# Optimization experiments

Hardware: AMD Instinct MI355X
Metric: run time of the kernel (lower is better)

Reference implementation:

```python
import jax, jax.numpy as jnp
import numpy as np
import math

B, Hs, Ws, C, NH, PP = 4, 32, 32, 1024, 16, 128
N = Hs * Ws
HD = C // NH
MAX_REL = 32
ROPE_THETA = 10000.0


def _gelu(t):
    return jax.nn.gelu(t, approximate=False)  # torch nn.GELU default (erf)


def _rope(x):
    # x: [B, nh, N, hd]; interleaved even/odd rotation as in _apply_rope
    hd = x.shape[-1]
    inv_freq = 1.0 / (ROPE_THETA ** (jnp.arange(0, hd, 2, dtype=jnp.float32) / hd))
    pos = jnp.arange(x.shape[-2], dtype=jnp.float32)
    ang = pos[:, None] * inv_freq[None, :]  # [N, hd/2]
    sin, cos = jnp.sin(ang), jnp.cos(ang)
    x1, x2 = x[..., 0::2], x[..., 1::2]
    return jnp.stack([x1 * cos - x2 * sin, x2 * cos + x1 * sin], axis=-1).reshape(x.shape)


def _rel_bias(table):
    # static index computation (numpy), gather from learned table -> [1, NH, N, N]
    coords = np.arange(Hs)
    cy, cx = np.meshgrid(coords, coords, indexing='ij')
    cf = np.stack([cy.reshape(-1), cx.reshape(-1)])  # [2, N]
    rel = cf[:, :, None] - cf[:, None, :]            # [2, N, N]
    idx = (rel[0] + MAX_REL - 1) * (2 * MAX_REL - 1) + (rel[1] + MAX_REL - 1)
    return table[jnp.asarray(idx.reshape(-1))].reshape(N, N, NH).transpose(2, 0, 1)[None]


def setup_inputs() -> dict:
    key = jax.random.key(0)
    ks = iter(jax.random.split(key, 40))
    def w(shape, s=0.02):
        return jax.random.normal(next(ks), shape, jnp.float32) * s
    return dict(
        x=jax.random.normal(next(ks), (B, N, C), jnp.float32),
        plucker=jax.random.normal(next(ks), (B, Hs, Ws, 6), jnp.float32),
        w_qkv=w((C, 3 * C)), w_self_proj=w((C, C)), b_self_proj=jnp.zeros((C,), jnp.float32),
        pl_w1=w((6, 2 * PP)), pl_b1=jnp.zeros((2 * PP,), jnp.float32),
        pl_w2=w((2 * PP, PP)), pl_b2=jnp.zeros((PP,), jnp.float32),
        pl_w3=w((PP, PP)), pl_b3=jnp.zeros((PP,), jnp.float32),
        w_cq=w((C, C)), w_pk=w((PP, C)), w_pv=w((PP, C)),
        w_cross_proj=w((C, C)), b_cross_proj=jnp.zeros((C,), jnp.float32),
        ray_dir_bias=w((NH,)),
        ds_w1=w((6, 4 * NH)), ds_b1=jnp.zeros((4 * NH,), jnp.float32),
        ds_w2=w((4 * NH, NH)), ds_b2=jnp.zeros((NH,), jnp.float32),
        gb_w1=w((2 * PP, C // 2)), gb_b1=jnp.zeros((C // 2,), jnp.float32),
        gb_w2=w((C // 2, NH)), gb_b2=jnp.zeros((NH,), jnp.float32),
        rel_table=w(((2 * MAX_REL - 1) ** 2, NH)),
        gfe_w1=w((C + PP, C)), gfe_b1=jnp.zeros((C,), jnp.float32),
        gfe_w2=w((C, C)), gfe_b2=jnp.zeros((C,), jnp.float32),
    )


def reference(x, plucker, w_qkv, w_self_proj, b_self_proj,
              pl_w1, pl_b1, pl_w2, pl_b2, pl_w3, pl_b3,
              w_cq, w_pk, w_pv, w_cross_proj, b_cross_proj,
              ray_dir_bias, ds_w1, ds_b1, ds_w2, ds_b2,
              gb_w1, gb_b1, gb_w2, gb_b2, rel_table,
              gfe_w1, gfe_b1, gfe_w2, gfe_b2):
    scale = HD ** (-0.5)
    pl_flat = plucker.reshape(B, N, 6)

    # ---- self attention with RoPE + relative position bias ----
    qkv = (x @ w_qkv).reshape(B, N, 3, NH, HD).transpose(2, 0, 3, 1, 4)
    q, k, v = qkv[0], qkv[1], qkv[2]          # [B, NH, N, HD]
    q, k = _rope(q), _rope(k)
    attn = jnp.einsum('bhnd,bhmd->bhnm', q, k) * scale + _rel_bias(rel_table)
    attn = jax.nn.softmax(attn, axis=-1)
    sa = jnp.einsum('bhnm,bhmd->bhnd', attn, v).transpose(0, 2, 1, 3).reshape(B, N, C)
    sa = sa @ w_self_proj + b_self_proj

    # ---- plucker mlp embedding ----
    pp = _gelu(pl_flat @ pl_w1 + pl_b1)
    pp = _gelu(pp @ pl_w2 + pl_b2)
    pp = pp @ pl_w3 + pl_b3                   # [B, N, PP]

    # ---- cross attention (features -> plucker) with geometric biases ----
    cq = (sa @ w_cq).reshape(B, N, NH, HD).transpose(0, 2, 1, 3)
    ck = (pp @ w_pk).reshape(B, N, NH, HD).transpose(0, 2, 1, 3)
    cv = (pp @ w_pv).reshape(B, N, NH, HD).transpose(0, 2, 1, 3)
    cq, ck = _rope(cq), _rope(ck)
    ca = jnp.einsum('bhnd,bhmd->bhnm', cq, ck) * scale

    # ray direction similarity bias (per-head learned weight)
    d = pl_flat[..., :3]
    dn = d / jnp.maximum(jnp.linalg.norm(d, axis=-1, keepdims=True), 1e-12)
    sim = jnp.einsum('bnd,bmd->bnm', dn, dn)  # [B, N, N]
    ca = ca + sim[:, None, :, :] * ray_dir_bias[None, :, None, None]

    # distance-aware per-query multiplicative scale
    ds = jnp.tanh(_gelu(pl_flat @ ds_w1 + ds_b1) @ ds_w2 + ds_b2)  # [B, N, NH]
    ca = ca * (1.0 + ds.transpose(0, 2, 1)[..., None])

    # geometric attention bias from spatial diffs of plucker features
    p2 = pp.reshape(B, Hs, Ws, PP)
    hdiff = jnp.pad(jnp.abs(p2[:, :, 1:] - p2[:, :, :-1]), ((0, 0), (0, 0), (0, 1), (0, 0)))
    vdiff = jnp.pad(jnp.abs(p2[:, 1:] - p2[:, :-1]), ((0, 0), (0, 1), (0, 0), (0, 0)))
    sd = jnp.concatenate([hdiff, vdiff], axis=-1).reshape(B, N, 2 * PP)
    gb = jnp.tanh(_gelu(sd @ gb_w1 + gb_b1) @ gb_w2 + gb_b2)  # [B, N, NH]
    ca = ca + gb.transpose(0, 2, 1)[:, :, None, :]            # broadcast over queries

    ca = jax.nn.softmax(ca, axis=-1)
    co = jnp.einsum('bhnm,bhmd->bhnd', ca, cv).transpose(0, 2, 1, 3).reshape(B, N, C)
    co = co @ w_cross_proj + b_cross_proj

    # ---- geometric feature enhancement + residual ----
    enh = _gelu(jnp.concatenate([co, pp], axis=-1) @ gfe_w1 + gfe_b1) @ gfe_w2 + gfe_b2
    return enh + x
```

## Files before the change

### kernel.cpp

```cpp
#include <hip/hip_runtime.h>
#include <math.h>

#define B_ 4
#define N_ 1024
#define C_ 1024
#define NH_ 16
#define HD_ 64
#define PP_ 128
#define LOG2E 1.4426950408889634f

typedef __bf16 bf16;
typedef __attribute__((ext_vector_type(8))) __bf16 bf16x8;
typedef __attribute__((ext_vector_type(4))) __bf16 bf16x4;
typedef __attribute__((ext_vector_type(4))) float f32x4;

#define MFMA_BF16(a, b, c) __builtin_amdgcn_mfma_f32_16x16x32_bf16((a), (b), (c), 0, 0, 0)

__device__ __forceinline__ float gelu_f(float x) {
    return 0.5f * x * (1.0f + erff(x * 0.70710678118654752f));
}

__device__ __forceinline__ void gload16(const void* g, void* l) {
    __builtin_amdgcn_global_load_lds(
        (const __attribute__((address_space(1))) void*)g,
        (__attribute__((address_space(3))) void*)l, 16, 0, 0);
}

__device__ __forceinline__ void stage64(const bf16* __restrict__ g, int pitchB,
                                        bf16* lds, int t) {
    int row = t >> 3, c = t & 7;
    const char* src = (const char*)g + (size_t)row * pitchB + ((c ^ (row & 7)) << 4);
    gload16(src, lds + (size_t)(t & 448) * 8);
}

__device__ __forceinline__ void stage32(const bf16* __restrict__ g, bf16* lds, int t) {
    if (t < 256) {
        int row = t >> 3, c = t & 7;
        const char* src = (const char*)g + (size_t)row * 128 + ((c ^ (row & 7)) << 4);
        gload16(src, lds + (size_t)(t & 192) * 8);
    }
}

__device__ __forceinline__ bf16x8 lds8_swz(const bf16* lds, int row, int colb) {
    return *reinterpret_cast<const bf16x8*>(
        (const char*)lds + row * 128 + (colb ^ ((row & 7) << 4)));
}

__device__ __forceinline__ bf16x8 lds8_swz256(const bf16* lds, int row, int colb) {
    return *reinterpret_cast<const bf16x8*>(
        (const char*)lds + row * 256 + (colb ^ ((row & 7) << 4)));
}

__device__ __forceinline__ bf16x8 lds8_ke(const bf16* lds, int kr, int g) {
    int r = kr >> 1;
    int ch = ((kr & 1) * 4 + g) ^ (r & 7);
    return *reinterpret_cast<const bf16x8*>((const char*)lds + r * 128 + (ch << 4));
}

__global__ __launch_bounds__(256) void tabs_k(const float* __restrict__ rel_table,
                                              float* __restrict__ relT,
                                              float2* __restrict__ rt)
{
    int g = blockIdx.x * 256 + threadIdx.x;
    if (g < 32768) {
        const int n = g >> 5, i = g & 31;
        const float inv = powf(10000.0f, -(float)(2 * i) / 64.0f);
        const float ang = (float)n * inv;
        rt[g] = make_float2(cosf(ang), sinf(ang));
    } else {
        int i = g - 32768;
        if (i < 16 * 3969) {
            int h = i / 3969, idx = i - h * 3969;
            relT[i] = rel_table[idx * 16 + h];
        }
    }
}

struct TJobs {
    const float* src[11];
    bf16* dst[11];
    int K[11];
    int N[11];
    int base[12];
};

__global__ __launch_bounds__(256) void tcast_k(TJobs J)
{
    int tile = blockIdx.x;
    int j = 0;
    while (j + 1 < 11 && tile >= J.base[j + 1]) ++j;
    tile -= J.base[j];
    const int Kd = J.K[j], Nd = J.N[j];
    const int ntx = Nd >> 5;
    const int n0 = (tile % ntx) * 32, k0 = (tile / ntx) * 32;
    __shared__ float tl[32][33];
    const int t = threadIdx.x, tx = t & 31, ty = t >> 5;
    const float* src = J.src[j];
    bf16* dst = J.dst[j];
    #pragma unroll
    for (int r = 0; r < 4; ++r) {
        int kk = ty + r * 8;
        tl[kk][tx] = src[(size_t)(k0 + kk) * Nd + n0 + tx];
    }
    __syncthreads();
    #pragma unroll
    for (int r = 0; r < 4; ++r) {
        int nn = ty + r * 8;
        dst[(size_t)(n0 + nn) * Kd + k0 + tx] = (bf16)tl[tx][nn];
    }
}

__global__ __launch_bounds__(256) void cast_rm(const float* __restrict__ in,
                                               bf16* __restrict__ out, int n4)
{
    int g = blockIdx.x * 256 + threadIdx.x;
    if (g >= n4) return;
    float4 v = reinterpret_cast<const float4*>(in)[g];
    bf16x4 o = {(bf16)v.x, (bf16)v.y, (bf16)v.z, (bf16)v.w};
    reinterpret_cast<bf16x4*>(out)[g] = o;
}

template<int NI, int BK>
__global__ __launch_bounds__(256) void gemm_m(
    const bf16* __restrict__ A, const bf16* __restrict__ A2,
    const bf16* __restrict__ Bt, const bf16* __restrict__ Bt2,
    const float* __restrict__ bias, const float* __restrict__ resid,
    void* __restrict__ out0, void* __restrict__ out1, void* __restrict__ out2,
    const float2* __restrict__ rtab,
    int M, int N, int K, int K1A, int K1B, int epi, int act_gelu, float scale)
{
    __shared__ bf16 As[2][128 * BK];
    __shared__ bf16 Bs[2][NI * 32 * BK];
    const int t = threadIdx.x;
    const int w = t >> 6, lane = t & 63;
    const int row0 = blockIdx.y * 128, col0 = blockIdx.x * (NI * 32);
    const int wm = w >> 1, wn = w & 1;
    const int K2A = K - K1A, K2B = K - K1B;
    f32x4 acc[4][NI];
    #pragma unroll
    for (int mi = 0; mi < 4; ++mi)
        #pragma unroll
        for (int ni = 0; ni < NI; ++ni)
            acc[mi][ni] = (f32x4){0.f, 0.f, 0.f, 0.f};

    #define STAGE_AB32(k0, buf)                                                \
        {                                                                      \
            _Pragma("unroll")                                                  \
            for (int r = 0; r < 2; ++r) {                                      \
                int c = r * 256 + t;                                           \
                int rr = c >> 2, koff = (c & 3) * 8;                           \
                const bf16* srca = ((k0) < K1A)                                \
                    ? A + (size_t)(row0 + rr) * K1A + (k0) + koff              \
                    : A2 + (size_t)(row0 + rr) * K2A + ((k0) - K1A) + koff;    \
                gload16(srca, As[buf] + (size_t)(r * 256 + (t & 192)) * 8);    \
            }                                                                  \
            _Pragma("unroll")                                                  \
            for (int r = 0; r < NI / 2; ++r) {                                 \
                int c = r * 256 + t;                                           \
                int rr = c >> 2, koff = (c & 3) * 8;                           \
                const bf16* srcb = ((k0) < K1B)                                \
                    ? Bt + (size_t)(col0 + rr) * K1B + (k0) + koff             \
                    : Bt2 + (size_t)(col0 + rr) * K2B + ((k0) - K1B) + koff;   \
                gload16(srcb, Bs[buf] + (size_t)(r * 256 + (t & 192)) * 8);    \
            }                                                                  \
        }

    #define STAGE_AB64(k0, buf)                                                \
        {                                                                      \
            const bf16* abase; int apitch;                                     \
            if ((k0) < K1A) { abase = A + (k0); apitch = K1A; }                \
            else            { abase = A2 + ((k0) - K1A); apitch = K2A; }       \
            _Pragma("unroll")                                                  \
            for (int r = 0; r < 4; ++r) {                                      \
                int c = r * 256 + t;                                           \
                int rr = c >> 3, cc = c & 7;                                   \
                const char* srca = (const char*)(abase + (size_t)(row0 + rr) * apitch) \
                                   + ((cc ^ (rr & 7)) << 4);                   \
                gload16(srca, As[buf] + (size_t)(r * 256 + (t & 192)) * 8);    \
            }                                                                  \
            const bf16* bbase; int bpitch;                                     \
            if ((k0) < K1B) { bbase = Bt + (k0); bpitch = K1B; }               \
            else            { bbase = Bt2 + ((k0) - K1B); bpitch = K2B; }      \
            _Pragma("unroll")                                                  \
            for (int r = 0; r < NI; ++r) {                                     \
                int c = r * 256 + t;                                           \
                int rr = c >> 3, cc = c & 7;                                   \
                const char* srcb = (const char*)(bbase + (size_t)(col0 + rr) * bpitch) \
                                   + ((cc ^ (rr & 7)) << 4);                   \
                gload16(srcb, Bs[buf] + (size_t)(r * 256 + (t & 192)) * 8);    \
            }                                                                  \
        }

    int cur = 0;
    const int nk = K / BK;
    if constexpr (BK == 32) {
        STAGE_AB32(0, 0);
        __syncthreads();
        for (int kk = 0; kk < nk; ++kk) {
            if (kk + 1 < nk) STAGE_AB32((kk + 1) * 32, cur ^ 1);
            bf16x8 af[4], bfv[NI];
            #pragma unroll
            for (int mi = 0; mi < 4; ++mi)
                af[mi] = *reinterpret_cast<const bf16x8*>(
                    As[cur] + (wm * 64 + mi * 16 + (lane & 15)) * 32 + (lane >> 4) * 8);
            #pragma unroll
            for (int ni = 0; ni < NI; ++ni)
                bfv[ni] = *reinterpret_cast<const bf16x8*>(
                    Bs[cur] + (wn * (NI * 16) + ni * 16 + (lane & 15)) * 32 + (lane >> 4) * 8);
            #pragma unroll
            for (int mi = 0; mi < 4; ++mi)
                #pragma unroll
                for (int ni = 0; ni < NI; ++ni)
                    acc[mi][ni] = MFMA_BF16(af[mi], bfv[ni], acc[mi][ni]);
            __syncthreads();
            cur ^= 1;
        }
    } else {
        STAGE_AB64(0, 0);
        __syncthreads();
        for (int kk = 0; kk < nk; ++kk) {
            if (kk + 1 < nk) STAGE_AB64((kk + 1) * 64, cur ^ 1);
            bf16x8 af[4][2], bfv[NI][2];
            #pragma unroll
            for (int mi = 0; mi < 4; ++mi)
                #pragma unroll
                for (int kh = 0; kh < 2; ++kh)
                    af[mi][kh] = lds8_swz(As[cur], wm * 64 + mi * 16 + (lane & 15),
                                          kh * 64 + (lane >> 4) * 16);
            #pragma unroll
            for (int ni = 0; ni < NI; ++ni)
                #pragma unroll
                for (int kh = 0; kh < 2; ++kh)
                    bfv[ni][kh] = lds8_swz(Bs[cur], wn * (NI * 16) + ni * 16 + (lane & 15),
                                           kh * 64 + (lane >> 4) * 16);
            #pragma unroll
            for (int kh = 0; kh < 2; ++kh)
                #pragma unroll
                for (int mi = 0; mi < 4; ++mi)
                    #pragma unroll
                    for (int ni = 0; ni < NI; ++ni)
                        acc[mi][ni] = MFMA_BF16(af[mi][kh], bfv[ni][kh], acc[mi][ni]);
            __syncthreads();
            cur ^= 1;
        }
    }
    #undef STAGE_AB32
    #undef STAGE_AB64

    #pragma unroll
    for (int mi = 0; mi < 4; ++mi) {
        #pragma unroll
        for (int ni = 0; ni < NI; ++ni) {
            const int col = col0 + wn * (NI * 16) + ni * 16 + (lane & 15);
            if (epi <= 1 || epi == 5) {
                const float bv = bias ? bias[col] : 0.f;
                #pragma unroll
                for (int j = 0; j < 4; ++j) {
                    const int row = row0 + wm * 64 + mi * 16 + (lane >> 4) * 4 + j;
                    float v = acc[mi][ni][j] + bv;
                    if (act_gelu) v = gelu_f(v);
                    if (epi == 0) {
                        if (resid) v += resid[(size_t)row * N + col];
                        ((float*)out0)[(size_t)row * N + col] = v;
                    } else if (epi == 1) {
                        ((bf16*)out0)[(size_t)row * N + col] = (bf16)v;
                    } else {
                        ((float*)out0)[(size_t)row * N + col] = v;
                        ((bf16*)out1)[(size_t)row * N + col] = (bf16)v;
                    }
                }
            } else if (epi == 2) {
                const int reg = col >> 10;
                const int h = (col >> 6) & 15, d = col & 63;
                if (reg <= 1) {
                    bf16* dst = reg == 0 ? (bf16*)out0 : (bf16*)out1;
                    const float sc = reg == 0 ? scale : 1.0f;
                    #pragma unroll
                    for (int j = 0; j < 4; ++j) {
                        const int row = row0 + wm * 64 + mi * 16 + (lane >> 4) * 4 + j;
                        const int b = row >> 10, n = row & 1023;
                        float v = acc[mi][ni][j];
                        float pv = __shfl_xor(v, 1);
                        float2 cs = rtab[(n << 5) + (d >> 1)];
                        float o = (d & 1) == 0 ? v * cs.x - pv * cs.y
                                               : v * cs.x + pv * cs.y;
                        dst[((size_t)((b * 16 + h) * 1024 + n)) * 64 + d] = (bf16)(o * sc);
                    }
                } else {
                    bf16x4 o4;
                    #pragma unroll
                    for (int j = 0; j < 4; ++j) o4[j] = (bf16)acc[mi][ni][j];
                    const int row = row0 + wm * 64 + mi * 16 + (lane >> 4) * 4;
                    const int b = row >> 10, n = row & 1023;
                    *reinterpret_cast<bf16x4*>(
                        (bf16*)out2 + ((size_t)((b * 16 + h) * 64 + d)) * 1024 + n) = o4;
                }
            } else if (epi == 3 || epi == 6) {
                const int h = (col >> 6) & 15, d = col & 63;
                const float bv = bias ? bias[col] : 0.f;
                #pragma unroll
                for (int j = 0; j < 4; ++j) {
                    const int row = row0 + wm * 64 + mi * 16 + (lane >> 4) * 4 + j;
                    const int b = row >> 10, n = row & 1023;
                    float v = acc[mi][ni][j] + bv;
                    float pv = __shfl_xor(v, 1);
                    float2 cs = rtab[(n << 5) + (d >> 1)];
                    float o = (d & 1) == 0 ? v * cs.x - pv * cs.y
                                           : v * cs.x + pv * cs.y;
                    float sc = scale;
                    if (epi == 6) sc *= 1.0f + resid[(size_t)row * 16 + h];
                    ((bf16*)out0)[((size_t)((b * 16 + h) * 1024 + n)) * 64 + d] = (bf16)(o * sc);
                }
            } else if (epi == 7) {
                const int reg = col >> 10;
                const int h = (col >> 6) & 15, d = col & 63;
                if (reg == 0) {
                    #pragma unroll
                    for (int j = 0; j < 4; ++j) {
                        const int row = row0 + wm * 64 + mi * 16 + (lane >> 4) * 4 + j;
                        const int b = row >> 10, n = row & 1023;
                        float v = acc[mi][ni][j];
                        float pv = __shfl_xor(v, 1);
                        float2 cs = rtab[(n << 5) + (d >> 1)];
                        float o = (d & 1) == 0 ? v * cs.x - pv * cs.y
                                               : v * cs.x + pv * cs.y;
                        ((bf16*)out0)[((size_t)((b * 16 + h) * 1024 + n)) * 64 + d] = (bf16)o;
                    }
                } else {
                    bf16x4 o4;
                    #pragma unroll
                    for (int j = 0; j < 4; ++j) o4[j] = (bf16)acc[mi][ni][j];
                    const int row = row0 + wm * 64 + mi * 16 + (lane >> 4) * 4;
                    const int b = row >> 10, n = row & 1023;
                    *reinterpret_cast<bf16x4*>(
                        (bf16*)out2 + ((size_t)((b * 16 + h) * 64 + d)) * 1024 + n) = o4;
                }
            } else {
                const int h = (col >> 6) & 15, d = col & 63;
                bf16x4 o4;
                #pragma unroll
                for (int j = 0; j < 4; ++j) o4[j] = (bf16)acc[mi][ni][j];
                const int row = row0 + wm * 64 + mi * 16 + (lane >> 4) * 4;
                const int b = row >> 10, n = row & 1023;
                *reinterpret_cast<bf16x4*>(
                    (bf16*)out0 + ((size_t)((b * 16 + h) * 64 + d)) * 1024 + n) = o4;
            }
        }
    }
}

__device__ __forceinline__ void attn_bid(int bid, int& bh, int& r0t) {
    const int xcd = bid & 7, s = bid >> 3;
    bh = (s >> 3) * 8 + xcd;
    r0t = s & 7;
}

__global__ __launch_bounds__(512) void attn_self_m(
    const bf16* __restrict__ qb, const bf16* __restrict__ kb, const bf16* __restrict__ vtb,
    const float* __restrict__ relT, bf16* __restrict__ sab)
{
    __shared__ bf16 Ks[2][64 * 64];
    __shared__ bf16 Vs[2][80 * 64];
    __shared__ bf16 Ps[128 * 64];
    __shared__ float relb[2][320];
    const int t = threadIdx.x, w = t >> 6, lane = t & 63;
    int bh, r0t;
    attn_bid(blockIdx.x, bh, r0t);
    const int b = bh >> 4, h = bh & 15, r0 = r0t * 128;
    const float* relTh = relT + h * 3969;
    const int y0 = r0 >> 5;

    {
        const bf16* g = qb + ((size_t)bh * 1024 + r0) * 64;
        #pragma unroll
        for (int r = 0; r < 2; ++r) {
            int i = r * 512 + t;
            int row = i >> 3, c = i & 7;
            const char* src = (const char*)g + (size_t)row * 128 + ((c ^ (row & 7)) << 4);
            gload16(src, Ps + (size_t)(r * 512 + (t & 448)) * 8);
        }
    }
    __syncthreads();
    bf16x8 aq[2];
    {
        const int qr = w * 16 + (lane & 15);
        aq[0] = lds8_swz(Ps, qr, (lane >> 4) * 16);
        aq[1] = lds8_swz(Ps, qr, 64 + (lane >> 4) * 16);
    }
    for (int i = t; i < 2048; i += 512) {
        int buf = i >> 10, idx = i & 1023;
        int row = 64 + (idx >> 6), col = idx & 63;
        Vs[buf][row * 64 + col] = (row == 64) ? (bf16)1.0f : (bf16)0.0f;
    }
    __syncthreads();
    stage64(kb + (size_t)bh * 65536, 128, Ks[0], t);
    stage64(vtb + (size_t)bh * 65536, 2048, Vs[0], t);
    if (t < 320) relb[0][t] = LOG2E * relTh[(y0 + 30 + (t >> 6)) * 63 + min(t & 63, 62)];

    float m_run[4];
    f32x4 of[4], ofe;
    #pragma unroll
    for (int j = 0; j < 4; ++j) m_run[j] = -3e38f;
    #pragma unroll
    for (int dt = 0; dt < 4; ++dt) of[dt] = (f32x4){0.f, 0.f, 0.f, 0.f};
    ofe = (f32x4){0.f, 0.f, 0.f, 0.f};

    const int qrow_lo = (lane >> 4) * 4;
    int dybase[4];
    #pragma unroll
    for (int j = 0; j < 4; ++j) {
        int qg = r0 + w * 16 + qrow_lo + j;
        dybase[j] = (((qg >> 5) - y0) + 1) * 64 + (qg & 31) + 31;
    }
    __syncthreads();

    int cur = 0;
    for (int mt = 0; mt < 16; ++mt) {
        if (mt < 15) {
            stage64(kb + (size_t)bh * 65536 + (size_t)(mt + 1) * 64 * 64, 128, Ks[cur ^ 1], t);
            stage64(vtb + (size_t)bh * 65536 + (size_t)(mt + 1) * 64, 2048, Vs[cur ^ 1], t);
            if (t < 320)
                relb[cur ^ 1][t] = LOG2E * relTh[(y0 - 2 * (mt + 1) + 30 + (t >> 6)) * 63 + min(t & 63, 62)];
        }
        f32x4 sf[4];
        __builtin_amdgcn_s_setprio(1);
        #pragma unroll
        for (int ct = 0; ct < 4; ++ct) {
            const int kr = ct * 16 + (lane & 15);
            f32x4 a = (f32x4){0.f, 0.f, 0.f, 0.f};
            a = MFMA_BF16(aq[0], lds8_swz(Ks[cur], kr, (lane >> 4) * 16), a);
            a = MFMA_BF16(aq[1], lds8_swz(Ks[cur], kr, 64 + (lane >> 4) * 16), a);
            sf[ct] = a;
        }
// ... 144 lines not shown
        f32x4 sf[4];
        __builtin_amdgcn_s_setprio(1);
        #pragma unroll
        for (int ct = 0; ct < 4; ++ct) {
            const int kr = ct * 16 + (lane & 15);
            f32x4 a = (f32x4){0.f, 0.f, 0.f, 0.f};
            a = MFMA_BF16(aq[0], lds8_swz(Ks[cur], kr, (lane >> 4) * 16), a);
            a = MFMA_BF16(aq[1], lds8_swz(Ks[cur], kr, 64 + (lane >> 4) * 16), a);
            a = MFMA_BF16(aqe, lds8_ke(Ke[cur], kr, lane >> 4), a);
            sf[ct] = a;
        }
        __builtin_amdgcn_s_setprio(0);
        float lmax[4];
        #pragma unroll
        for (int j = 0; j < 4; ++j)
            lmax[j] = fmaxf(fmaxf(sf[0][j], sf[1][j]), fmaxf(sf[2][j], sf[3][j]));
        bool need = false;
        #pragma unroll
        for (int j = 0; j < 4; ++j) need |= (lmax[j] > m_run[j] + 8.0f);
        if (__any(need)) {
            float mx[4], alpha[4];
            #pragma unroll
            for (int j = 0; j < 4; ++j) mx[j] = lmax[j];
            #pragma unroll
            for (int d = 1; d < 16; d <<= 1)
                #pragma unroll
                for (int j = 0; j < 4; ++j) mx[j] = fmaxf(mx[j], __shfl_xor(mx[j], d));
            #pragma unroll
            for (int j = 0; j < 4; ++j) {
                float mn = fmaxf(m_run[j], mx[j]);
                alpha[j] = exp2f(m_run[j] - mn);
                m_run[j] = mn;
            }
            #pragma unroll
            for (int dt = 0; dt < 4; ++dt)
                #pragma unroll
                for (int j = 0; j < 4; ++j) of[dt][j] *= alpha[j];
            #pragma unroll
            for (int j = 0; j < 4; ++j) ofe[j] *= alpha[j];
        }
        #pragma unroll
        for (int ct = 0; ct < 4; ++ct)
            #pragma unroll
            for (int j = 0; j < 4; ++j)
                sf[ct][j] = exp2f(sf[ct][j] - m_run[j]);
        #pragma unroll
        for (int ct = 0; ct < 4; ++ct)
            #pragma unroll
            for (int j = 0; j < 4; ++j) {
                const int prow = w * 16 + qrow_lo + j;
                const int ch = (ct * 2 + ((lane & 15) >> 3)) ^ (prow & 7);
                *reinterpret_cast<bf16*>((char*)Ps + prow * 128 + (ch << 4) + (lane & 7) * 2)
                    = (bf16)sf[ct][j];
            }
        asm volatile("s_waitcnt lgkmcnt(0)" ::: "memory");
        __builtin_amdgcn_sched_barrier(0);
        bf16x8 ap0 = lds8_swz(Ps, w * 16 + (lane & 15), (lane >> 4) * 16);
        bf16x8 ap1 = lds8_swz(Ps, w * 16 + (lane & 15), 64 + (lane >> 4) * 16);
        __builtin_amdgcn_s_setprio(1);
        #pragma unroll
        for (int dt = 0; dt < 4; ++dt) {
            const int vr = dt * 16 + (lane & 15);
            of[dt] = MFMA_BF16(ap0, lds8_swz(Vs[cur], vr, (lane >> 4) * 16), of[dt]);
            of[dt] = MFMA_BF16(ap1, lds8_swz(Vs[cur], vr, 64 + (lane >> 4) * 16), of[dt]);
        }
        {
            const int vr = 64 + (lane & 15);
            ofe = MFMA_BF16(ap0, lds8_swz(Vs[cur], vr, (lane >> 4) * 16), ofe);
            ofe = MFMA_BF16(ap1, lds8_swz(Vs[cur], vr, 64 + (lane >> 4) * 16), ofe);
        }
        __builtin_amdgcn_s_setprio(0);
        __syncthreads();
        cur ^= 1;
    }
    float inv[4];
    #pragma unroll
    for (int j = 0; j < 4; ++j) inv[j] = 1.f / __shfl(ofe[j], lane & 48);
    #pragma unroll
    for (int dt = 0; dt < 4; ++dt)
        #pragma unroll
        for (int j = 0; j < 4; ++j)
            cob[((size_t)(b * N_ + r0 + w * 16 + qrow_lo + j)) * C_ + h * 64 + dt * 16 + (lane & 15)] =
                (bf16)(of[dt][j] * inv[j]);
}

__global__ __launch_bounds__(256) void plucker1_k(
    const float* __restrict__ pl,
    const float* __restrict__ w1, const float* __restrict__ b1,
    const float* __restrict__ dw1, const float* __restrict__ db1,
    const float* __restrict__ dw2, const float* __restrict__ db2,
    bf16* __restrict__ h1b, float* __restrict__ ds, float* __restrict__ dn)
{
    const int t = threadIdx.x;
    __shared__ float plr[6];
    __shared__ float dh[64];
    #pragma unroll 1
    for (int rr = 0; rr < 4; ++rr) {
        const int row = blockIdx.x * 4 + rr;
        if (t < 6) plr[t] = pl[(size_t)row * 6 + t];
        __syncthreads();
        {
            float a = b1[t];
            #pragma unroll
            for (int j = 0; j < 6; ++j) a = fmaf(plr[j], w1[j * 256 + t], a);
            h1b[(size_t)row * 256 + t] = (bf16)gelu_f(a);
        }
        if (t < 64) {
            float d = db1[t];
            #pragma unroll
            for (int j = 0; j < 6; ++j) d = fmaf(plr[j], dw1[j * 64 + t], d);
            dh[t] = gelu_f(d);
        }
        if (t == 0) {
            float x = plr[0], y = plr[1], z = plr[2];
            float nrm = fmaxf(sqrtf(x * x + y * y + z * z), 1e-12f);
            dn[(size_t)row * 4 + 0] = x / nrm;
            dn[(size_t)row * 4 + 1] = y / nrm;
            dn[(size_t)row * 4 + 2] = z / nrm;
            dn[(size_t)row * 4 + 3] = 0.f;
        }
        __syncthreads();
        if (t < 16) {
            float d = db2[t];
            #pragma unroll 8
            for (int j = 0; j < 64; ++j) d = fmaf(dh[j], dw2[j * 16 + t], d);
            ds[(size_t)row * 16 + t] = tanhf(d);
        }
        __syncthreads();
    }
}

__global__ __launch_bounds__(256) void pl23m_k(
    const bf16* __restrict__ h1, const bf16* __restrict__ w2T, const float* __restrict__ b2,
    const bf16* __restrict__ w3T, const float* __restrict__ b3,
    float* __restrict__ pp, bf16* __restrict__ ppb)
{
    __shared__ bf16 Am[64 * 128];
    __shared__ bf16 Wm[128 * 128];
    const int t = threadIdx.x, w = t >> 6, lane = t & 63;
    const int row0 = blockIdx.x * 64;
    f32x4 acc[8];
    #pragma unroll
    for (int nt = 0; nt < 8; ++nt) acc[nt] = (f32x4){0.f, 0.f, 0.f, 0.f};

    for (int kc = 0; kc < 2; ++kc) {
        #pragma unroll
        for (int r = 0; r < 4; ++r) {
            int i = r * 256 + t;
            int row = i >> 4, c = i & 15;
            const char* src = (const char*)(h1 + (size_t)(row0 + row) * 256 + kc * 128)
                              + ((c ^ (row & 7)) << 4);
            gload16(src, Am + (size_t)(r * 256 + (t & 192)) * 8);
        }
        #pragma unroll
        for (int r = 0; r < 8; ++r) {
            int i = r * 256 + t;
            int row = i >> 4, c = i & 15;
            const char* src = (const char*)(w2T + (size_t)row * 256 + kc * 128)
                              + ((c ^ (row & 7)) << 4);
            gload16(src, Wm + (size_t)(r * 256 + (t & 192)) * 8);
        }
        __syncthreads();
        #pragma unroll
        for (int step = 0; step < 4; ++step) {
            bf16x8 af = lds8_swz256(Am, w * 16 + (lane & 15), step * 64 + (lane >> 4) * 16);
            #pragma unroll
            for (int nt = 0; nt < 8; ++nt) {
                bf16x8 bfv = lds8_swz256(Wm, nt * 16 + (lane & 15), step * 64 + (lane >> 4) * 16);
                acc[nt] = MFMA_BF16(af, bfv, acc[nt]);
            }
        }
        __syncthreads();
    }
    #pragma unroll
    for (int r = 0; r < 8; ++r) {
        int i = r * 256 + t;
        int row = i >> 4, c = i & 15;
        const char* src = (const char*)(w3T + (size_t)row * 128) + ((c ^ (row & 7)) << 4);
        gload16(src, Wm + (size_t)(r * 256 + (t & 192)) * 8);
    }
    #pragma unroll
    for (int nt = 0; nt < 8; ++nt) {
        const int col = nt * 16 + (lane & 15);
        const float bv = b2[col];
        #pragma unroll
        for (int j = 0; j < 4; ++j) {
            const int row = w * 16 + (lane >> 4) * 4 + j;
            const int byte = row * 256 + (((col * 2) & ~15) ^ ((row & 7) << 4)) + ((col * 2) & 15);
            *reinterpret_cast<bf16*>((char*)Am + byte) = (bf16)gelu_f(acc[nt][j] + bv);
        }
    }
    __syncthreads();
    f32x4 acc2[8];
    #pragma unroll
    for (int nt = 0; nt < 8; ++nt) acc2[nt] = (f32x4){0.f, 0.f, 0.f, 0.f};
    #pragma unroll
    for (int step = 0; step < 4; ++step) {
        bf16x8 af = lds8_swz256(Am, w * 16 + (lane & 15), step * 64 + (lane >> 4) * 16);
        #pragma unroll
        for (int nt = 0; nt < 8; ++nt) {
            bf16x8 bfv = lds8_swz256(Wm, nt * 16 + (lane & 15), step * 64 + (lane >> 4) * 16);
            acc2[nt] = MFMA_BF16(af, bfv, acc2[nt]);
        }
    }
    #pragma unroll
    for (int nt = 0; nt < 8; ++nt) {
        const int col = nt * 16 + (lane & 15);
        const float bv = b3[col];
        #pragma unroll
        for (int j = 0; j < 4; ++j) {
            const int row = row0 + w * 16 + (lane >> 4) * 4 + j;
            const float v = acc2[nt][j] + bv;
// ... 66 lines not shown
    const float* pl_b3 = (const float*)d_in[10];
    const float* w_cq  = (const float*)d_in[11];
    const float* w_pk  = (const float*)d_in[12];
    const float* w_pv  = (const float*)d_in[13];
    const float* w_cp  = (const float*)d_in[14];
    const float* b_cp  = (const float*)d_in[15];
    const float* rdb   = (const float*)d_in[16];
    const float* ds_w1 = (const float*)d_in[17];
    const float* ds_b1 = (const float*)d_in[18];
    const float* ds_w2 = (const float*)d_in[19];
    const float* ds_b2 = (const float*)d_in[20];
    const float* gb_w1 = (const float*)d_in[21];
    const float* gb_b1 = (const float*)d_in[22];
    const float* gb_w2 = (const float*)d_in[23];
    const float* gb_b2 = (const float*)d_in[24];
    const float* rel_t = (const float*)d_in[25];
    const float* gfw1  = (const float*)d_in[26];
    const float* gfb1  = (const float*)d_in[27];
    const float* gfw2  = (const float*)d_in[28];
    const float* gfb2  = (const float*)d_in[29];

    char* W = (char*)d_ws;
    float* out = (float*)d_out;
    const size_t MB = 1ull << 20;
    const size_t KB = 1024;

    bf16* qb     = (bf16*)(W + 0);
    bf16* kb     = (bf16*)(W + 8 * MB);
    bf16* vtb    = (bf16*)(W + 16 * MB);
    bf16* cqb    = qb;
    bf16* ckb    = kb;
    bf16* cvtb   = vtb;
    bf16* xb     = (bf16*)(W + 24 * MB);
    bf16* wqkvT  = (bf16*)(W + 32 * MB);
    bf16* wspT   = (bf16*)(W + 38 * MB);
    bf16* wcqT   = (bf16*)(W + 40 * MB);
    bf16* wpkT   = (bf16*)(W + 42 * MB);
    bf16* wpvT   = (bf16*)(W + 42 * MB + 256 * KB);
    bf16* wcpT   = (bf16*)(W + 43 * MB);
    bf16* gfw1T  = (bf16*)(W + 45 * MB);
    bf16* gfw2T  = (bf16*)(W + 48 * MB);
    bf16* gbw1T  = (bf16*)(W + 50 * MB);
    bf16* plw2T  = (bf16*)(W + 50 * MB + 256 * KB);
    bf16* plw3T  = (bf16*)(W + 50 * MB + 320 * KB);
    bf16* sab    = (bf16*)(W + 51 * MB);
    bf16* cob    = sab;
    bf16* sapb   = (bf16*)(W + 59 * MB);
    bf16* copb   = sapb;
    float* pp    = (float*)(W + 67 * MB);
    bf16* ppb    = (bf16*)(W + 69 * MB);
    bf16* sdb16  = (bf16*)(W + 70 * MB);
    bf16* h1b    = (bf16*)(W + 72 * MB);
    bf16* gbh    = (bf16*)(W + 75 * MB);
    float* dsb   = (float*)(W + 79 * MB);
    float* dnb   = (float*)(W + 79 * MB + 256 * KB);
    float2* rtab = (float2*)(W + 80 * MB);
    float* relTb = (float*)(W + 80 * MB + 256 * KB);
    bf16* hidb   = (bf16*)(W + 81 * MB);
    bf16* qeb    = (bf16*)(W + 89 * MB);
    bf16* keb    = (bf16*)(W + 93 * MB);

    const dim3 blk(256);

    TJobs J;
    J.src[0] = w_qkv; J.dst[0] = wqkvT; J.K[0] = 1024; J.N[0] = 3072;
    J.src[1] = w_sp;  J.dst[1] = wspT;  J.K[1] = 1024; J.N[1] = 1024;
    J.src[2] = w_cq;  J.dst[2] = wcqT;  J.K[2] = 1024; J.N[2] = 1024;
    J.src[3] = w_pk;  J.dst[3] = wpkT;  J.K[3] = 128;  J.N[3] = 1024;
    J.src[4] = w_pv;  J.dst[4] = wpvT;  J.K[4] = 128;  J.N[4] = 1024;
    J.src[5] = w_cp;  J.dst[5] = wcpT;  J.K[5] = 1024; J.N[5] = 1024;
    J.src[6] = gfw1;  J.dst[6] = gfw1T; J.K[6] = 1152; J.N[6] = 1024;
    J.src[7] = gfw2;  J.dst[7] = gfw2T; J.K[7] = 1024; J.N[7] = 1024;
    J.src[8] = gb_w1; J.dst[8] = gbw1T; J.K[8] = 256;  J.N[8] = 512;
    J.src[9] = pl_w2; J.dst[9] = plw2T; J.K[9] = 256;  J.N[9] = 128;
    J.src[10]= pl_w3; J.dst[10]= plw3T; J.K[10]= 128;  J.N[10]= 128;
    {
        int acc = 0;
        for (int j = 0; j < 11; ++j) {
            J.base[j] = acc;
            acc += (J.N[j] >> 5) * (J.K[j] >> 5);
        }
        J.base[11] = acc;
    }
    tcast_k<<<J.base[11], blk, 0, stream>>>(J);
    cast_rm<<<4096, blk, 0, stream>>>(x, xb, 1048576);
    tabs_k<<<377, blk, 0, stream>>>(rel_t, relTb, rtab);

    gemm_m<2, 64><<<dim3(48, 32), blk, 0, stream>>>(xb, nullptr, wqkvT, nullptr, nullptr, nullptr,
        qb, kb, vtb, rtab, 4096, 3072, 1024, 1024, 1024, 2, 0, 0.125f * LOG2E);
    attn_self_m<<<512, dim3(512), 0, stream>>>(qb, kb, vtb, relTb, sab);
    gemm_m<2, 64><<<dim3(16, 32), blk, 0, stream>>>(sab, nullptr, wspT, nullptr, b_sp, nullptr,
        sapb, nullptr, nullptr, nullptr, 4096, 1024, 1024, 1024, 1024, 1, 0, 1.f);
    plucker1_k<<<1024, blk, 0, stream>>>(pl, pl_w1, pl_b1,
                                         ds_w1, ds_b1, ds_w2, ds_b2, h1b, dsb, dnb);
    pl23m_k<<<64, blk, 0, stream>>>(h1b, plw2T, pl_b2, plw3T, pl_b3, pp, ppb);
    sd_k<<<2048, blk, 0, stream>>>(pp, sdb16);
    gemm_m<2, 64><<<dim3(8, 32), blk, 0, stream>>>(sdb16, nullptr, gbw1T, nullptr, gb_b1, nullptr,
        gbh, nullptr, nullptr, nullptr, 4096, 512, 256, 256, 256, 1, 1, 1.f);
    gb2x_k<<<256, blk, 0, stream>>>(gbh, gb_w2, gb_b2, dnb, dsb, rdb, qeb, keb);
    gemm_m<2, 64><<<dim3(16, 32), blk, 0, stream>>>(sapb, nullptr, wcqT, nullptr, nullptr, dsb,
        cqb, nullptr, nullptr, rtab, 4096, 1024, 1024, 1024, 1024, 6, 0, 0.125f * LOG2E);
    gemm_m<2, 64><<<dim3(32, 32), blk, 0, stream>>>(ppb, nullptr, wpkT, nullptr, nullptr, nullptr,
        ckb, nullptr, cvtb, rtab, 4096, 2048, 128, 128, 128, 7, 0, 1.f);
    attn_cross_m<<<512, dim3(512), 0, stream>>>(cqb, qeb, ckb, keb, cvtb, cob);
    gemm_m<2, 64><<<dim3(16, 32), blk, 0, stream>>>(cob, nullptr, wcpT, nullptr, b_cp, nullptr,
        copb, nullptr, nullptr, nullptr, 4096, 1024, 1024, 1024, 1024, 1, 0, 1.f);
    gemm_m<2, 64><<<dim3(16, 32), blk, 0, stream>>>(copb, ppb, gfw1T, nullptr, gfb1, nullptr,
        hidb, nullptr, nullptr, nullptr, 4096, 1024, 1152, 1024, 1152, 1, 1, 1.f);
    gemm_m<2, 64><<<dim3(16, 32), blk, 0, stream>>>(hidb, nullptr, gfw2T, nullptr, gfb2, x,
        out, nullptr, nullptr, nullptr, 4096, 1024, 1024, 1024, 1024, 0, 0, 1.f);
}
```

Measured before the change: 325.6 us.

## Merge preprocessing kernels and co-launch independent GEMMs in shared grids

Fuses the weight transpose-cast, x cast, table construction and plucker MLP into one multi-role pre-kernel. Independent GEMM pairs (geometric-bias first layer with self projection, and cross-query with key/value projection) are merged into single launches with a split block index. The launch order is rearranged so small plucker kernels run before self-attention. This cuts launch count and lets small GEMMs fill the device alongside larger ones, at the cost of one fixed 48KB shared buffer for every GEMM role.

```diff
diff --git a/kernel.cpp b/kernel.cpp
--- a/kernel.cpp
+++ b/kernel.cpp
@@ -57,25 +57,6 @@
     return *reinterpret_cast<const bf16x8*>((const char*)lds + r * 128 + (ch << 4));
 }
 
-__global__ __launch_bounds__(256) void tabs_k(const float* __restrict__ rel_table,
-                                              float* __restrict__ relT,
-                                              float2* __restrict__ rt)
-{
-    int g = blockIdx.x * 256 + threadIdx.x;
-    if (g < 32768) {
-        const int n = g >> 5, i = g & 31;
-        const float inv = powf(10000.0f, -(float)(2 * i) / 64.0f);
-        const float ang = (float)n * inv;
-        rt[g] = make_float2(cosf(ang), sinf(ang));
-    } else {
-        int i = g - 32768;
-        if (i < 16 * 3969) {
-            int h = i / 3969, idx = i - h * 3969;
-            relT[i] = rel_table[idx * 16 + h];
-        }
-    }
-}
-
 struct TJobs {
     const float* src[11];
     bf16* dst[11];
@@ -84,86 +65,134 @@
     int base[12];
 };
 
-__global__ __launch_bounds__(256) void tcast_k(TJobs J)
+__global__ __launch_bounds__(256) void pre_k(
+    TJobs J, const float* __restrict__ x, bf16* __restrict__ xb,
+    const float* __restrict__ rel_table, float* __restrict__ relT, float2* __restrict__ rt,
+    const float* __restrict__ pl,
+    const float* __restrict__ w1, const float* __restrict__ b1,
+    const float* __restrict__ dw1, const float* __restrict__ db1,
+    const float* __restrict__ dw2, const float* __restrict__ db2,
+    bf16* __restrict__ h1b, float* __restrict__ ds, float* __restrict__ dn)
 {
-    int tile = blockIdx.x;
-    int j = 0;
-    while (j + 1 < 11 && tile >= J.base[j + 1]) ++j;
-    tile -= J.base[j];
-    const int Kd = J.K[j], Nd = J.N[j];
-    const int ntx = Nd >> 5;
-    const int n0 = (tile % ntx) * 32, k0 = (tile / ntx) * 32;
     __shared__ float tl[32][33];
-    const int t = threadIdx.x, tx = t & 31, ty = t >> 5;
-    const float* src = J.src[j];
-    bf16* dst = J.dst[j];
-    #pragma unroll
-    for (int r = 0; r < 4; ++r) {
-        int kk = ty + r * 8;
-        tl[kk][tx] = src[(size_t)(k0 + kk) * Nd + n0 + tx];
-    }
-    __syncthreads();
-    #pragma unroll
-    for (int r = 0; r < 4; ++r) {
-        int nn = ty + r * 8;
-        dst[(size_t)(n0 + nn) * Kd + k0 + tx] = (bf16)tl[tx][nn];
-    }
-}
-
-__global__ __launch_bounds__(256) void cast_rm(const float* __restrict__ in,
-                                               bf16* __restrict__ out, int n4)
+    __shared__ float plr[6];
+    __shared__ float dh[64];
+    const int t = threadIdx.x;
+    const int bid = blockIdx.x;
+    const int ntc = J.base[11];
+    if (bid < ntc) {
+        int tile = bid;
+        int j = 0;
+        while (j + 1 < 11 && tile >= J.base[j + 1]) ++j;
+        tile -= J.base[j];
+        const int Kd = J.K[j], Nd = J.N[j];
+        const int ntx = Nd >> 5;
+        const int n0 = (tile % ntx) * 32, k0 = (tile / ntx) * 32;
+        const int tx = t & 31, ty = t >> 5;
+        const float* src = J.src[j];
+        bf16* dst = J.dst[j];
+        #pragma unroll
+        for (int r = 0; r < 4; ++r) {
+            int kk = ty + r * 8;
+            tl[kk][tx] = src[(size_t)(k0 + kk) * Nd + n0 + tx];
+        }
+        __syncthreads();
+        #pragma unroll
+        for (int r = 0; r < 4; ++r) {
+            int nn = ty + r * 8;
+            dst[(size_t)(n0 + nn) * Kd + k0 + tx] = (bf16)tl[tx][nn];
+        }
+    } else if (bid < ntc + 4096) {
+        int g = (bid - ntc) * 256 + t;
+        float4 v = reinterpret_cast<const float4*>(x)[g];
+        bf16x4 o = {(bf16)v.x, (bf16)v.y, (bf16)v.z, (bf16)v.w};
+        reinterpret_cast<bf16x4*>(xb)[g] = o;
+    } else if (bid < ntc + 4096 + 377) {
+        int g = (bid - ntc - 4096) * 256 + t;
+        if (g < 32768) {
+            const int n = g >> 5, i = g & 31;
+            const float inv = powf(10000.0f, -(float)(2 * i) / 64.0f);
+            const float ang = (float)n * inv;
+            rt[g] = make_float2(cosf(ang), sinf(ang));
+        } else {
+            int i = g - 32768;
+            if (i < 16 * 3969) {
+                int h = i / 3969, idx = i - h * 3969;
+                relT[i] = rel_table[idx * 16 + h];
+            }
+        }
+    } else {
+        const int pb = bid - ntc - 4096 - 377;
+        #pragma unroll 1
+        for (int rr = 0; rr < 4; ++rr) {
+            const int row = pb * 4 + rr;
+            if (t < 6) plr[t] = pl[(size_t)row * 6 + t];
+            __syncthreads();
+            {
+                float a = b1[t];
+                #pragma unroll
+                for (int j = 0; j < 6; ++j) a = fmaf(plr[j], w1[j * 256 + t], a);
+                h1b[(size_t)row * 256 + t] = (bf16)gelu_f(a);
+            }
+            if (t < 64) {
+                float d = db1[t];
+                #pragma unroll
+                for (int j = 0; j < 6; ++j) d = fmaf(plr[j], dw1[j * 64 + t], d);
+                dh[t] = gelu_f(d);
+            }
+            if (t == 0) {
+                float xx = plr[0], yy = plr[1], zz = plr[2];
+                float nrm = fmaxf(sqrtf(xx * xx + yy * yy + zz * zz), 1e-12f);
+                dn[(size_t)row * 4 + 0] = xx / nrm;
+                dn[(size_t)row * 4 + 1] = yy / nrm;
+                dn[(size_t)row * 4 + 2] = zz / nrm;
+                dn[(size_t)row * 4 + 3] = 0.f;
+            }
+            __syncthreads();
+            if (t < 16) {
+                float d = db2[t];
+                #pragma unroll 8
+                for (int j = 0; j < 64; ++j) d = fmaf(dh[j], dw2[j * 16 + t], d);
+                ds[(size_t)row * 16 + t] = tanhf(d);
+            }
+            __syncthreads();
+        }
+    }
+}
+
+struct GJob {
+    const bf16* A; const bf16* A2; const bf16* Bt; const bf16* Bt2;
+    const float* bias; const float* resid;
+    void* out0; void* out1; void* out2;
+    const float2* rtab;
+    int N, K, K1A, K1B, epi, act_gelu, gx;
+    float scale;
+};
+
+__device__ __forceinline__ void gemm_body(const GJob& P, int bx, int by, char* smem)
 {
-    int g = blockIdx.x * 256 + threadIdx.x;
-    if (g >= n4) return;
-    float4 v = reinterpret_cast<const float4*>(in)[g];
-    bf16x4 o = {(bf16)v.x, (bf16)v.y, (bf16)v.z, (bf16)v.w};
-    reinterpret_cast<bf16x4*>(out)[g] = o;
-}
-
-template<int NI, int BK>
-__global__ __launch_bounds__(256) void gemm_m(
-    const bf16* __restrict__ A, const bf16* __restrict__ A2,
-    const bf16* __restrict__ Bt, const bf16* __restrict__ Bt2,
-    const float* __restrict__ bias, const float* __restrict__ resid,
-    void* __restrict__ out0, void* __restrict__ out1, void* __restrict__ out2,
-    const float2* __restrict__ rtab,
-    int M, int N, int K, int K1A, int K1B, int epi, int act_gelu, float scale)
-{
-    __shared__ bf16 As[2][128 * BK];
-    __shared__ bf16 Bs[2][NI * 32 * BK];
+    const bf16* A = P.A; const bf16* A2 = P.A2;
+    const bf16* Bt = P.Bt; const bf16* Bt2 = P.Bt2;
+    const float* bias = P.bias; const float* resid = P.resid;
+    void* out0 = P.out0; void* out1 = P.out1; void* out2 = P.out2;
+    const float2* rtab = P.rtab;
+    const int N = P.N, K = P.K, K1A = P.K1A, K1B = P.K1B;
+    const int epi = P.epi, act_gelu = P.act_gelu;
+    const float scale = P.scale;
+
+    bf16 (*As)[128 * 64] = (bf16(*)[128 * 64])smem;
+    bf16 (*Bs)[64 * 64]  = (bf16(*)[64 * 64])(smem + 32768);
     const int t = threadIdx.x;
     const int w = t >> 6, lane = t & 63;
-    const int row0 = blockIdx.y * 128, col0 = blockIdx.x * (NI * 32);
+    const int row0 = by * 128, col0 = bx * 64;
     const int wm = w >> 1, wn = w & 1;
     const int K2A = K - K1A, K2B = K - K1B;
-    f32x4 acc[4][NI];
+    f32x4 acc[4][2];
     #pragma unroll
     for (int mi = 0; mi < 4; ++mi)
         #pragma unroll
-        for (int ni = 0; ni < NI; ++ni)
+        for (int ni = 0; ni < 2; ++ni)
             acc[mi][ni] = (f32x4){0.f, 0.f, 0.f, 0.f};
-
-    #define STAGE_AB32(k0, buf)                                                \
-        {                                                                      \
-            _Pragma("unroll")                                                  \
-            for (int r = 0; r < 2; ++r) {                                      \
-                int c = r * 256 + t;                                           \
-                int rr = c >> 2, koff = (c & 3) * 8;                           \
-                const bf16* srca = ((k0) < K1A)                                \
-                    ? A + (size_t)(row0 + rr) * K1A + (k0) + koff              \
-                    : A2 + (size_t)(row0 + rr) * K2A + ((k0) - K1A) + koff;    \
-                gload16(srca, As[buf] + (size_t)(r * 256 + (t & 192)) * 8);    \
-            }                                                                  \
-            _Pragma("unroll")                                                  \
-            for (int r = 0; r < NI / 2; ++r) {                                 \
-                int c = r * 256 + t;                                           \
-                int rr = c >> 2, koff = (c & 3) * 8;                           \
-                const bf16* srcb = ((k0) < K1B)                                \
-                    ? Bt + (size_t)(col0 + rr) * K1B + (k0) + koff             \
-                    : Bt2 + (size_t)(col0 + rr) * K2B + ((k0) - K1B) + koff;   \
-                gload16(srcb, Bs[buf] + (size_t)(r * 256 + (t & 192)) * 8);    \
-            }                                                                  \
-        }
 
     #define STAGE_AB64(k0, buf)                                                \
         {                                                                      \
@@ -182,7 +211,7 @@
             if ((k0) < K1B) { bbase = Bt + (k0); bpitch = K1B; }               \
             else            { bbase = Bt2 + ((k0) - K1B); bpitch = K2B; }      \
             _Pragma("unroll")                                                  \
-            for (int r = 0; r < NI; ++r) {                                     \
+            for (int r = 0; r < 2; ++r) {                                      \
                 int c = r * 256 + t;                                           \
                 int rr = c >> 3, cc = c & 7;                                   \
                 const char* srcb = (const char*)(bbase + (size_t)(col0 + rr) * bpitch) \
@@ -192,66 +221,41 @@
         }
 
     int cur = 0;
-    const int nk = K / BK;
-    if constexpr (BK == 32) {
-        STAGE_AB32(0, 0);
-        __syncthreads();
-        for (int kk = 0; kk < nk; ++kk) {
-            if (kk + 1 < nk) STAGE_AB32((kk + 1) * 32, cur ^ 1);
-            bf16x8 af[4], bfv[NI];
-            #pragma unroll
-            for (int mi = 0; mi < 4; ++mi)
-                af[mi] = *reinterpret_cast<const bf16x8*>(
-                    As[cur] + (wm * 64 + mi * 16 + (lane & 15)) * 32 + (lane >> 4) * 8);
-            #pragma unroll
-            for (int ni = 0; ni < NI; ++ni)
-                bfv[ni] = *reinterpret_cast<const bf16x8*>(
-                    Bs[cur] + (wn * (NI * 16) + ni * 16 + (lane & 15)) * 32 + (lane >> 4) * 8);
+    const int nk = K >> 6;
+    STAGE_AB64(0, 0);
+    __syncthreads();
+    for (int kk = 0; kk < nk; ++kk) {
+        if (kk + 1 < nk) STAGE_AB64((kk + 1) * 64, cur ^ 1);
+        bf16x8 af[4][2], bfv[2][2];
+        #pragma unroll
+        for (int mi = 0; mi < 4; ++mi)
+            #pragma unroll
+            for (int kh = 0; kh < 2; ++kh)
+                af[mi][kh] = lds8_swz(As[cur], wm * 64 + mi * 16 + (lane & 15),
+                                      kh * 64 + (lane >> 4) * 16);
+        #pragma unroll
+        for (int ni = 0; ni < 2; ++ni)
+            #pragma unroll
+            for (int kh = 0; kh < 2; ++kh)
+                bfv[ni][kh] = lds8_swz(Bs[cur], wn * 32 + ni * 16 + (lane & 15),
+                                       kh * 64 + (lane >> 4) * 16);
+        #pragma unroll
+        for (int kh = 0; kh < 2; ++kh)
             #pragma unroll
             for (int mi = 0; mi < 4; ++mi)
                 #pragma unroll
-                for (int ni = 0; ni < NI; ++ni)
-                    acc[mi][ni] = MFMA_BF16(af[mi], bfv[ni], acc[mi][ni]);
-            __syncthreads();
-            cur ^= 1;
-        }
-    } else {
-        STAGE_AB64(0, 0);
+                for (int ni = 0; ni < 2; ++ni)
+                    acc[mi][ni] = MFMA_BF16(af[mi][kh], bfv[ni][kh], acc[mi][ni]);
         __syncthreads();
-        for (int kk = 0; kk < nk; ++kk) {
-            if (kk + 1 < nk) STAGE_AB64((kk + 1) * 64, cur ^ 1);
-            bf16x8 af[4][2], bfv[NI][2];
-            #pragma unroll
-            for (int mi = 0; mi < 4; ++mi)
-                #pragma unroll
-                for (int kh = 0; kh < 2; ++kh)
-                    af[mi][kh] = lds8_swz(As[cur], wm * 64 + mi * 16 + (lane & 15),
-                                          kh * 64 + (lane >> 4) * 16);
-            #pragma unroll
-            for (int ni = 0; ni < NI; ++ni)
-                #pragma unroll
-                for (int kh = 0; kh < 2; ++kh)
-                    bfv[ni][kh] = lds8_swz(Bs[cur], wn * (NI * 16) + ni * 16 + (lane & 15),
-                                           kh * 64 + (lane >> 4) * 16);
-            #pragma unroll
-            for (int kh = 0; kh < 2; ++kh)
-                #pragma unroll
-                for (int mi = 0; mi < 4; ++mi)
-                    #pragma unroll
-                    for (int ni = 0; ni < NI; ++ni)
-                        acc[mi][ni] = MFMA_BF16(af[mi][kh], bfv[ni][kh], acc[mi][ni]);
-            __syncthreads();
-            cur ^= 1;
-        }
-    }
-    #undef STAGE_AB32
+        cur ^= 1;
+    }
     #undef STAGE_AB64
 
     #pragma unroll
     for (int mi = 0; mi < 4; ++mi) {
         #pragma unroll
-        for (int ni = 0; ni < NI; ++ni) {
-            const int col = col0 + wn * (NI * 16) + ni * 16 + (lane & 15);
+        for (int ni = 0; ni < 2; ++ni) {
+            const int col = col0 + wn * 32 + ni * 16 + (lane & 15);
             if (epi <= 1 || epi == 5) {
                 const float bv = bias ? bias[col] : 0.f;
                 #pragma unroll
@@ -349,6 +353,23 @@
     }
 }
 
+__global__ __launch_bounds__(256) void gemm_k(GJob P)
+{
+    __shared__ char smem[49152];
+    gemm_body(P, blockIdx.x % P.gx, blockIdx.x / P.gx, smem);
+}
+
+__global__ __launch_bounds__(256) void gemm2_k(GJob P0, GJob P1, int split)
+{
+    __shared__ char smem[49152];
+    int id = blockIdx.x;
+    if (id < split) gemm_body(P0, id % P0.gx, id / P0.gx, smem);
+    else {
+        id -= split;
+        gemm_body(P1, id % P1.gx, id / P1.gx, smem);
+    }
+}
+
 __device__ __forceinline__ void attn_bid(int bid, int& bh, int& r0t) {
     const int xcd = bid & 7, s = bid >> 3;
     bh = (s >> 3) * 8 + xcd;
@@ -659,52 +680,6 @@
         for (int j = 0; j < 4; ++j)
             cob[((size_t)(b * N_ + r0 + w * 16 + qrow_lo + j)) * C_ + h * 64 + dt * 16 + (lane & 15)] =
                 (bf16)(of[dt][j] * inv[j]);
-}
-
-__global__ __launch_bounds__(256) void plucker1_k(
-    const float* __restrict__ pl,
-    const float* __restrict__ w1, const float* __restrict__ b1,
-    const float* __restrict__ dw1, const float* __restrict__ db1,
-    const float* __restrict__ dw2, const float* __restrict__ db2,
-    bf16* __restrict__ h1b, float* __restrict__ ds, float* __restrict__ dn)
-{
-    const int t = threadIdx.x;
-    __shared__ float plr[6];
-    __shared__ float dh[64];
-    #pragma unroll 1
-    for (int rr = 0; rr < 4; ++rr) {
-        const int row = blockIdx.x * 4 + rr;
-        if (t < 6) plr[t] = pl[(size_t)row * 6 + t];
-        __syncthreads();
-        {
-            float a = b1[t];
-            #pragma unroll
-            for (int j = 0; j < 6; ++j) a = fmaf(plr[j], w1[j * 256 + t], a);
-            h1b[(size_t)row * 256 + t] = (bf16)gelu_f(a);
-        }
-        if (t < 64) {
-            float d = db1[t];
-            #pragma unroll
-            for (int j = 0; j < 6; ++j) d = fmaf(plr[j], dw1[j * 64 + t], d);
-            dh[t] = gelu_f(d);
-        }
-        if (t == 0) {
-            float x = plr[0], y = plr[1], z = plr[2];
-            float nrm = fmaxf(sqrtf(x * x + y * y + z * z), 1e-12f);
-            dn[(size_t)row * 4 + 0] = x / nrm;
-            dn[(size_t)row * 4 + 1] = y / nrm;
-            dn[(size_t)row * 4 + 2] = z / nrm;
-            dn[(size_t)row * 4 + 3] = 0.f;
-        }
-        __syncthreads();
-        if (t < 16) {
-            float d = db2[t];
-            #pragma unroll 8
-            for (int j = 0; j < 64; ++j) d = fmaf(dh[j], dw2[j * 16 + t], d);
-            ds[(size_t)row * 16 + t] = tanhf(d);
-        }
-        __syncthreads();
-    }
 }
 
 __global__ __launch_bounds__(256) void pl23m_k(
@@ -937,31 +912,47 @@
         }
         J.base[11] = acc;
     }
-    tcast_k<<<J.base[11], blk, 0, stream>>>(J);
-    cast_rm<<<4096, blk, 0, stream>>>(x, xb, 1048576);
-    tabs_k<<<377, blk, 0, stream>>>(rel_t, relTb, rtab);
-
-    gemm_m<2, 64><<<dim3(48, 32), blk, 0, stream>>>(xb, nullptr, wqkvT, nullptr, nullptr, nullptr,
-        qb, kb, vtb, rtab, 4096, 3072, 1024, 1024, 1024, 2, 0, 0.125f * LOG2E);
-    attn_self_m<<<512, dim3(512), 0, stream>>>(qb, kb, vtb, relTb, sab);
-    gemm_m<2, 64><<<dim3(16, 32), blk, 0, stream>>>(sab, nullptr, wspT, nullptr, b_sp, nullptr,
-        sapb, nullptr, nullptr, nullptr, 4096, 1024, 1024, 1024, 1024, 1, 0, 1.f);
-    plucker1_k<<<1024, blk, 0, stream>>>(pl, pl_w1, pl_b1,
-                                         ds_w1, ds_b1, ds_w2, ds_b2, h1b, dsb, dnb);
+    const int pre_blocks = J.base[11] + 4096 + 377 + 1024;
+
+    auto mkjob = [](const bf16* A, const bf16* A2, const bf16* Bt, const bf16* Bt2,
+                    const float* bias, const float* resid,
+                    void* o0, void* o1, void* o2, const float2* rt,
+                    int N, int K, int K1A, int K1B, int epi, int ag, int gx, float sc) {
+        GJob g;
+        g.A = A; g.A2 = A2; g.Bt = Bt; g.Bt2 = Bt2; g.bias = bias; g.resid = resid;
+        g.out0 = o0; g.out1 = o1; g.out2 = o2; g.rtab = rt;
+        g.N = N; g.K = K; g.K1A = K1A; g.K1B = K1B; g.epi = epi; g.act_gelu = ag;
+        g.gx = gx; g.scale = sc;
+        return g;
+    };
+
+    pre_k<<<pre_blocks, blk, 0, stream>>>(J, x, xb, rel_t, relTb, rtab,
+        pl, pl_w1, pl_b1, ds_w1, ds_b1, ds_w2, ds_b2, h1b, dsb, dnb);
+    GJob jqkv = mkjob(xb, nullptr, wqkvT, nullptr, nullptr, nullptr,
+                      qb, kb, vtb, rtab, 3072, 1024, 1024, 1024, 2, 0, 48, 0.125f * LOG2E);
+    gemm_k<<<1536, blk, 0, stream>>>(jqkv);
     pl23m_k<<<64, blk, 0, stream>>>(h1b, plw2T, pl_b2, plw3T, pl_b3, pp, ppb);
     sd_k<<<2048, blk, 0, stream>>>(pp, sdb16);
-    gemm_m<2, 64><<<dim3(8, 32), blk, 0, stream>>>(sdb16, nullptr, gbw1T, nullptr, gb_b1, nullptr,
-        gbh, nullptr, nullptr, nullptr, 4096, 512, 256, 256, 256, 1, 1, 1.f);
+    attn_self_m<<<512, dim3(512), 0, stream>>>(qb, kb, vtb, relTb, sab);
+    GJob jgb1 = mkjob(sdb16, nullptr, gbw1T, nullptr, gb_b1, nullptr,
+                      gbh, nullptr, nullptr, nullptr, 512, 256, 256, 256, 1, 1, 8, 1.f);
+    GJob jsp  = mkjob(sab, nullptr, wspT, nullptr, b_sp, nullptr,
+                      sapb, nullptr, nullptr, nullptr, 1024, 1024, 1024, 1024, 1, 0, 16, 1.f);
+    gemm2_k<<<256 + 512, blk, 0, stream>>>(jgb1, jsp, 256);
     gb2x_k<<<256, blk, 0, stream>>>(gbh, gb_w2, gb_b2, dnb, dsb, rdb, qeb, keb);
-    gemm_m<2, 64><<<dim3(16, 32), blk, 0, stream>>>(sapb, nullptr, wcqT, nullptr, nullptr, dsb,
-        cqb, nullptr, nullptr, rtab, 4096, 1024, 1024, 1024, 1024, 6, 0, 0.125f * LOG2E);
-    gemm_m<2, 64><<<dim3(32, 32), blk, 0, stream>>>(ppb, nullptr, wpkT, nullptr, nullptr, nullptr,
-        ckb, nullptr, cvtb, rtab, 4096, 2048, 128, 128, 128, 7, 0, 1.f);
+    GJob jcq  = mkjob(sapb, nullptr, wcqT, nullptr, nullptr, dsb,
+                      cqb, nullptr, nullptr, rtab, 1024, 1024, 1024, 1024, 6, 0, 16, 0.125f * LOG2E);
+    GJob jkcv = mkjob(ppb, nullptr, wpkT, nullptr, nullptr, nullptr,
+                      ckb, nullptr, cvtb, rtab, 2048, 128, 128, 128, 7, 0, 32, 1.f);
+    gemm2_k<<<512 + 1024, blk, 0, stream>>>(jcq, jkcv, 512);
     attn_cross_m<<<512, dim3(512), 0, stream>>>(cqb, qeb, ckb, keb, cvtb, cob);
-    gemm_m<2, 64><<<dim3(16, 32), blk, 0, stream>>>(cob, nullptr, wcpT, nullptr, b_cp, nullptr,
-        copb, nullptr, nullptr, nullptr, 4096, 1024, 1024, 1024, 1024, 1, 0, 1.f);
-    gemm_m<2, 64><<<dim3(16, 32), blk, 0, stream>>>(copb, ppb, gfw1T, nullptr, gfb1, nullptr,
-        hidb, nullptr, nullptr, nullptr, 4096, 1024, 1152, 1024, 1152, 1, 1, 1.f);
-    gemm_m<2, 64><<<dim3(16, 32), blk, 0, stream>>>(hidb, nullptr, gfw2T, nullptr, gfb2, x,
-        out, nullptr, nullptr, nullptr, 4096, 1024, 1024, 1024, 1024, 0, 0, 1.f);
-}
+    GJob jcp = mkjob(cob, nullptr, wcpT, nullptr, b_cp, nullptr,
+                     copb, nullptr, nullptr, nullptr, 1024, 1024, 1024, 1024, 1, 0, 16, 1.f);
+    gemm_k<<<512, blk, 0, stream>>>(jcp);
+    GJob jg1 = mkjob(copb, ppb, gfw1T, nullptr, gfb1, nullptr,
+                     hidb, nullptr, nullptr, nullptr, 1024, 1152, 1024, 1152, 1, 1, 16, 1.f);
+    gemm_k<<<512, blk, 0, stream>>>(jg1);
+    GJob jg2 = mkjob(hidb, nullptr, gfw2T, nullptr, gfb2, x,
+                     out, nullptr, nullptr, nullptr, 1024, 1024, 1024, 1024, 0, 0, 16, 1.f);
+    gemm_k<<<512, blk, 0, stream>>>(jg2);
+}
```

Measured after the change: 318.8 us. 2.1% less time.
